# Kernel optimization log

Measured on AMD Instinct MI355X. Metric: run time of the kernel, lower is better.

Reference implementation:

```python
import jax, jax.numpy as jnp
import numpy as np

D_MODEL = 2048
N_HEADS = 16
D_K = D_MODEL // N_HEADS
D_FF = ((int(D_MODEL * 8 / 3) + 63) // 64) * 64  # 5504
B, S = 2, 2048
EPS = 1e-6


def setup_inputs() -> dict:
    key = jax.random.key(0)
    ks = jax.random.split(key, 16)
    sc = 0.02
    x = jax.random.normal(ks[0], (B, S, D_MODEL), dtype=jnp.float32)
    mask = jnp.tril(jnp.ones((S, S), dtype=jnp.int32))[None]  # [1,S,S] causal
    inp = {
        'x': x,
        'mask': mask,
        'wq': jax.random.normal(ks[1], (D_MODEL, D_MODEL), jnp.float32) * sc,
        'bq': jnp.zeros((D_MODEL,), jnp.float32),
        'wk': jax.random.normal(ks[2], (D_MODEL, D_MODEL), jnp.float32) * sc,
        'bk': jnp.zeros((D_MODEL,), jnp.float32),
        'wv': jax.random.normal(ks[3], (D_MODEL, D_MODEL), jnp.float32) * sc,
        'bv': jnp.zeros((D_MODEL,), jnp.float32),
        'wo': jax.random.normal(ks[4], (D_MODEL, D_MODEL), jnp.float32) * sc,
        'bo': jnp.zeros((D_MODEL,), jnp.float32),
        'g1': jnp.ones((D_MODEL,), jnp.float32),  # RMSNorm weights
        'g2': jnp.ones((D_MODEL,), jnp.float32),
        'w1': jax.random.normal(ks[5], (D_MODEL, D_FF), jnp.float32) * sc,
        'w3': jax.random.normal(ks[6], (D_MODEL, D_FF), jnp.float32) * sc,
        'w2': jax.random.normal(ks[7], (D_FF, D_MODEL), jnp.float32) * sc,
    }
    return inp


def _rmsnorm(x, w):
    rms = jnp.sqrt(jnp.mean(x * x, axis=-1, keepdims=True) + EPS)
    return x / rms * w


def _block(x, mask, wq, bq, wk, bk, wv, bv, wo, bo, g1, g2, w1, w2, w3):
    b, s, _ = x.shape
    # --- attention sublayer (pre-LN) ---
    n = _rmsnorm(x, g1)
    q = (n @ wq + bq).reshape(b, s, N_HEADS, D_K).transpose(0, 2, 1, 3)
    k = (n @ wk + bk).reshape(b, s, N_HEADS, D_K).transpose(0, 2, 1, 3)
    v = (n @ wv + bv).reshape(b, s, N_HEADS, D_K).transpose(0, 2, 1, 3)
    scores = jnp.einsum('bhqd,bhkd->bhqk', q, k) / jnp.sqrt(jnp.float32(D_K))
    m = mask[:, None, :, :]  # [1,1,S,S]
    scores = jnp.where(m == 0, jnp.float32(-jnp.inf), scores)
    attn = jax.nn.softmax(scores, axis=-1)
    ao = jnp.einsum('bhqk,bhkd->bhqd', attn, v)
    ao = ao.transpose(0, 2, 1, 3).reshape(b, s, D_MODEL)
    x = x + (ao @ wo + bo)
    # --- SwiGLU FFN sublayer (pre-LN) ---
    n = _rmsnorm(x, g2)
    ffn = (jax.nn.silu(n @ w1) * (n @ w3)) @ w2
    return x + ffn


def reference(x, mask, wq, bq, wk, bk, wv, bv, wo, bo, g1, g2, w1, w2, w3):
    return _block(x, mask, wq, bq, wk, bk, wv, bv, wo, bo, g1, g2, w1, w2, w3)
```

## Files before the change

kernel.cpp:

```cpp
#include <hip/hip_runtime.h>
#include <stdint.h>

typedef unsigned short u16;
typedef __bf16 bf16x8 __attribute__((ext_vector_type(8)));
typedef float f32x4 __attribute__((ext_vector_type(4)));

#define D_MODEL 2048
#define NHEADS 16
#define DK 128
#define DFF 5504
#define DFFP 5632
#define BB 2
#define SS 2048
#define MTOK 4096
#define DQKV 6144

#define AS1 __attribute__((address_space(1)))
#define AS3 __attribute__((address_space(3)))

__device__ __forceinline__ u16 f2bf(float f){
  union { float f; uint32_t u; } v; v.f = f;
  uint32_t r = v.u + 0x7fffu + ((v.u >> 16) & 1u);
  return (u16)(r >> 16);
}
__device__ __forceinline__ float bf2f(u16 u){
  union { uint32_t u; float f; } v; v.u = ((uint32_t)u) << 16;
  return v.f;
}
__device__ __forceinline__ u16 cvt_bf16(float f){
  union { __bf16 h; u16 u; } v; v.h = (__bf16)f; return v.u;
}
__device__ __forceinline__ float fexp2(float x){
#if __has_builtin(__builtin_amdgcn_exp2f)
  return __builtin_amdgcn_exp2f(x);
#else
  return exp2f(x);
#endif
}

__global__ __launch_bounds__(256) void k_transpose_w(const float* __restrict__ W,
                                                     u16* __restrict__ Wt, int K, int Nsrc){
  __shared__ float tile[32][33];
  int n0 = blockIdx.x * 32, k0 = blockIdx.y * 32;
  int tx = threadIdx.x, ty = threadIdx.y;
  #pragma unroll
  for (int r = 0; r < 4; ++r){
    int n = n0 + tx;
    tile[ty + r*8][tx] = (n < Nsrc) ? W[(size_t)(k0 + ty + r*8) * Nsrc + n] : 0.0f;
  }
  __syncthreads();
  #pragma unroll
  for (int r = 0; r < 4; ++r)
    Wt[(size_t)(n0 + ty + r*8) * K + k0 + tx] = f2bf(tile[tx][ty + r*8]);
}

__global__ __launch_bounds__(256) void k_transpose_v(const u16* __restrict__ V,
                                                     u16* __restrict__ Vt, int ld){
  __shared__ u16 tile[32][33];
  int s0 = blockIdx.x * 32;
  int bh = blockIdx.y >> 2, dt = blockIdx.y & 3;
  int b = bh >> 4, h = bh & 15;
  int tx = threadIdx.x, ty = threadIdx.y;
  #pragma unroll
  for (int r = 0; r < 4; ++r)
    tile[ty + r*8][tx] = V[(size_t)(b*SS + s0 + ty + r*8) * ld + h*DK + dt*32 + tx];
  __syncthreads();
  #pragma unroll
  for (int r = 0; r < 4; ++r)
    Vt[(size_t)(bh*DK + dt*32 + ty + r*8) * SS + s0 + tx] = tile[tx][ty + r*8];
}

__global__ __launch_bounds__(256) void k_concat3(const float* __restrict__ a,
                                                 const float* __restrict__ b,
                                                 const float* __restrict__ c,
                                                 float* __restrict__ o){
  int i = blockIdx.x*256 + threadIdx.x;
  if (i >= DQKV) return;
  o[i] = (i < 2048) ? a[i] : (i < 4096 ? b[i-2048] : c[i-4096]);
}

__global__ __launch_bounds__(256) void k_rmsnorm(const float* __restrict__ X,
                                                 const float* __restrict__ g,
                                                 u16* __restrict__ out){
  int row = blockIdx.x, tid = threadIdx.x;
  const float* x = X + (size_t)row * D_MODEL;
  float4 a = ((const float4*)x)[tid*2];
  float4 b = ((const float4*)x)[tid*2+1];
  float ss = a.x*a.x + a.y*a.y + a.z*a.z + a.w*a.w
           + b.x*b.x + b.y*b.y + b.z*b.z + b.w*b.w;
  #pragma unroll
  for (int m = 1; m < 64; m <<= 1) ss += __shfl_xor(ss, m, 64);
  __shared__ float red[4];
  if ((tid & 63) == 0) red[tid >> 6] = ss;
  __syncthreads();
  float tot = red[0] + red[1] + red[2] + red[3];
  float sc = rsqrtf(tot * (1.0f / D_MODEL) + 1e-6f);
  float4 ga = ((const float4*)g)[tid*2];
  float4 gb = ((const float4*)g)[tid*2+1];
  uint32_t w0 = f2bf(a.x*sc*ga.x) | ((uint32_t)f2bf(a.y*sc*ga.y) << 16);
  uint32_t w1 = f2bf(a.z*sc*ga.z) | ((uint32_t)f2bf(a.w*sc*ga.w) << 16);
  uint32_t w2 = f2bf(b.x*sc*gb.x) | ((uint32_t)f2bf(b.y*sc*gb.y) << 16);
  uint32_t w3 = f2bf(b.z*sc*gb.z) | ((uint32_t)f2bf(b.w*sc*gb.w) << 16);
  ((uint4*)(out + (size_t)row * D_MODEL))[tid] = make_uint4(w0, w1, w2, w3);
}

__global__ __launch_bounds__(256) void k_silu_mul(const u16* __restrict__ a,
                                                  const u16* __restrict__ b,
                                                  u16* __restrict__ o, int n8){
  int i = blockIdx.x * 256 + threadIdx.x;
  if (i >= n8) return;
  uint4 av = ((const uint4*)a)[i];
  uint4 bv = ((const uint4*)b)[i];
  uint32_t aa[4] = {av.x, av.y, av.z, av.w};
  uint32_t bb[4] = {bv.x, bv.y, bv.z, bv.w};
  uint32_t rr[4];
  #pragma unroll
  for (int j = 0; j < 4; ++j){
    float x0 = bf2f((u16)(aa[j] & 0xffff)), x1 = bf2f((u16)(aa[j] >> 16));
    float y0 = bf2f((u16)(bb[j] & 0xffff)), y1 = bf2f((u16)(bb[j] >> 16));
    float r0 = x0 / (1.f + __expf(-x0)) * y0;
    float r1 = x1 / (1.f + __expf(-x1)) * y1;
    rr[j] = f2bf(r0) | ((uint32_t)f2bf(r1) << 16);
  }
  ((uint4*)o)[i] = make_uint4(rr[0], rr[1], rr[2], rr[3]);
}

__global__ __launch_bounds__(256) void k_add2(float* __restrict__ out,
                                              const float* __restrict__ p0,
                                              const float* __restrict__ p1, int n4){
  int stride = gridDim.x * 256;
  for (int i = blockIdx.x * 256 + threadIdx.x; i < n4; i += stride){
    float4 o = ((const float4*)out)[i];
    float4 a = ((const float4*)p0)[i];
    float4 b = ((const float4*)p1)[i];
    o.x += a.x + b.x; o.y += a.y + b.y; o.z += a.z + b.z; o.w += a.w + b.w;
    ((float4*)out)[i] = o;
  }
}

template<int EPI>
__global__ __launch_bounds__(512, 2) void k_gemm8p(
    const u16* __restrict__ A, const u16* __restrict__ Bt,
    const float* __restrict__ bias, const u16* __restrict__ aux,
    void* __restrict__ Cout, int M, int N, int K,
    int lda, int ldb, int ldc)
{
  extern __shared__ __align__(16) char smem[];
  const int tid = threadIdx.x;
  const int lane = tid & 63, wid = tid >> 6;
  const int wr = wid >> 2, wc = wid & 3;
  const int lrow = lane & 15, lhi = lane >> 4;

  int nwg = gridDim.x, wg = blockIdx.x;
  int ksl = 0;
  if constexpr (EPI == 6){
    int hn = nwg >> 1;
    if (wg >= hn){ ksl = 1; wg -= hn; }
    nwg = hn;
    A  += (size_t)ksl * K;
    Bt += (size_t)ksl * K;
  }

  int nbx = N >> 8, nbm = M >> 8;
  int xcd = wg & 7, sub = wg >> 3;
  int m0, n0;
  if ((nwg & 7) == 0 && (nbm & 1) == 0 && (nbx & 3) == 0){
    int mh = nbm >> 1;
    int mr = sub % mh, nc = sub / mh;
    m0 = (((xcd & 1) * mh) + mr) << 8;
    n0 = (((xcd >> 1) * (nbx >> 2)) + nc) << 8;
  } else {
    int qq = nwg >> 3, rr2 = nwg & 7;
    int swz = (xcd < rr2 ? xcd*(qq+1) : rr2*(qq+1) + (xcd-rr2)*qq) + sub;
    m0 = (swz / nbx) << 8; n0 = (swz % nbx) << 8;
  }

  const int nk = K >> 6;
  const int hA = wr, hB = wc >> 1;
  const int gA = wc;
  const int gB = (wr << 1) | (wc & 1);

  auto stA = [&](int d, int kk, int q){
    #pragma unroll
    for (int L = 0; L < 2; ++L){
      int p = q*8192 + gA*2048 + L*1024 + lane*16;
      int row = p >> 7;
      int o = (p & 127) ^ ((row & 7) << 4);
      __builtin_amdgcn_global_load_lds(
        (const AS1 void*)(A + (size_t)(m0 + hA*128 + row)*lda + kk + (o >> 1)),
        (AS3 void*)(smem + d*65536 + hA*16384 + p), 16, 0, 0);
    }
  };
  auto stB = [&](int d, int kk, int s){
    #pragma unroll
    for (int L = 0; L < 2; ++L){
      int p = s*4096 + (gB >> 1)*8192 + (gB & 1)*2048 + L*1024 + lane*16;
      int row = p >> 7;
      int o = (p & 127) ^ ((row & 7) << 4);
      __builtin_amdgcn_global_load_lds(
        (const AS1 void*)(Bt + (size_t)(n0 + hB*128 + row)*ldb + kk + (o >> 1)),
        (AS3 void*)(smem + d*65536 + 32768 + hB*16384 + p), 16, 0, 0);
    }
  };
  auto rdA = [&](int d, int rloc, int ks)->bf16x8{
    int p = rloc*128 + ((ks*64 + lhi*16) ^ ((rloc & 7) << 4));
    return *(const bf16x8*)(smem + d*65536 + hA*16384 + p);
  };
  auto rdB = [&](int d, int rloc, int ks)->bf16x8{
    int p = rloc*128 + ((ks*64 + lhi*16) ^ ((rloc & 7) << 4));
    return *(const bf16x8*)(smem + d*65536 + 32768 + hB*16384 + p);
  };

  f32x4 acc[8][4] = {};

  stA(0, 0, 0); stB(0, 0, 0); stB(0, 0, 1); stA(0, 0, 1);
  asm volatile("s_waitcnt vmcnt(0)" ::: "memory");
  __builtin_amdgcn_s_barrier();

  for (int t = 0; t < nk; ++t){
    int d = t & 1, dn = d ^ 1, kkn = (t + 1) << 6;
    bool pf = (t + 1 < nk);
    bf16x8 aR[8], bQ0[4], bQ1[4];

    #pragma unroll
    for (int ii = 0; ii < 4; ++ii){
      aR[ii*2]   = rdA(d, ii*16 + lrow, 0);
      aR[ii*2+1] = rdA(d, ii*16 + lrow, 1);
    }
    #pragma unroll
    for (int j = 0; j < 2; ++j){
      bQ0[j*2]   = rdB(d, (wc&1)*64 + j*16 + lrow, 0);
      bQ0[j*2+1] = rdB(d, (wc&1)*64 + j*16 + lrow, 1);
    }
    if (pf){ stA(dn, kkn, 0); stB(dn, kkn, 0); }
    __builtin_amdgcn_s_barrier();
    asm volatile("s_waitcnt lgkmcnt(0)" ::: "memory");
    __builtin_amdgcn_sched_barrier(0);
    __builtin_amdgcn_s_setprio(1);
    #pragma unroll
    for (int ii = 0; ii < 4; ++ii)
      #pragma unroll
      for (int j = 0; j < 2; ++j){
        acc[ii][j] = __builtin_amdgcn_mfma_f32_16x16x32_bf16(aR[ii*2],   bQ0[j*2],   acc[ii][j], 0, 0, 0);
        acc[ii][j] = __builtin_amdgcn_mfma_f32_16x16x32_bf16(aR[ii*2+1], bQ0[j*2+1], acc[ii][j], 0, 0, 0);
      }
    __builtin_amdgcn_s_setprio(0);
    if (pf) asm volatile("s_waitcnt vmcnt(6)" ::: "memory");
    else    asm volatile("s_waitcnt vmcnt(2)" ::: "memory");
    __builtin_amdgcn_sched_barrier(0);
    __builtin_amdgcn_s_barrier();

    #pragma unroll
    for (int j = 0; j < 2; ++j){
      bQ1[j*2]   = rdB(d, (wc&1)*64 + 32 + j*16 + lrow, 0);
      bQ1[j*2+1] = rdB(d, (wc&1)*64 + 32 + j*16 + lrow, 1);
    }
    if (pf) stB(dn, kkn, 1);
    __builtin_amdgcn_s_barrier();
    asm volatile("s_waitcnt lgkmcnt(0)" ::: "memory");
    __builtin_amdgcn_sched_barrier(0);
    __builtin_amdgcn_s_setprio(1);
    #pragma unroll
    for (int ii = 0; ii < 4; ++ii)
      #pragma unroll
      for (int j = 0; j < 2; ++j){
        acc[ii][2+j] = __builtin_amdgcn_mfma_f32_16x16x32_bf16(aR[ii*2],   bQ1[j*2],   acc[ii][2+j], 0, 0, 0);
        acc[ii][2+j] = __builtin_amdgcn_mfma_f32_16x16x32_bf16(aR[ii*2+1], bQ1[j*2+1], acc[ii][2+j], 0, 0, 0);
      }
    __builtin_amdgcn_s_setprio(0);
    if (pf) asm volatile("s_waitcnt vmcnt(6)" ::: "memory");
    else    asm volatile("s_waitcnt vmcnt(0)" ::: "memory");
    __builtin_amdgcn_sched_barrier(0);
    __builtin_amdgcn_s_barrier();

    #pragma unroll
    for (int ii = 0; ii < 4; ++ii){
      aR[ii*2]   = rdA(d, 64 + ii*16 + lrow, 0);
      aR[ii*2+1] = rdA(d, 64 + ii*16 + lrow, 1);
    }
    if (pf) stA(dn, kkn, 1);
    __builtin_amdgcn_s_barrier();
    asm volatile("s_waitcnt lgkmcnt(0)" ::: "memory");
    __builtin_amdgcn_sched_barrier(0);
    __builtin_amdgcn_s_setprio(1);
    #pragma unroll
    for (int ii = 0; ii < 4; ++ii)
      #pragma unroll
      for (int j = 0; j < 2; ++j){
        acc[4+ii][2+j] = __builtin_amdgcn_mfma_f32_16x16x32_bf16(aR[ii*2],   bQ1[j*2],   acc[4+ii][2+j], 0, 0, 0);
        acc[4+ii][2+j] = __builtin_amdgcn_mfma_f32_16x16x32_bf16(aR[ii*2+1], bQ1[j*2+1], acc[4+ii][2+j], 0, 0, 0);
      }
    __builtin_amdgcn_s_setprio(0);
    __builtin_amdgcn_s_barrier();

    __builtin_amdgcn_s_setprio(1);
    #pragma unroll
    for (int ii = 0; ii < 4; ++ii)
      #pragma unroll
      for (int j = 0; j < 2; ++j){
        acc[4+ii][j] = __builtin_amdgcn_mfma_f32_16x16x32_bf16(aR[ii*2],   bQ0[j*2],   acc[4+ii][j], 0, 0, 0);
        acc[4+ii][j] = __builtin_amdgcn_mfma_f32_16x16x32_bf16(aR[ii*2+1], bQ0[j*2+1], acc[4+ii][j], 0, 0, 0);
      }
    __builtin_amdgcn_s_setprio(0);
    if (pf) asm volatile("s_waitcnt vmcnt(4)" ::: "memory");
    __builtin_amdgcn_sched_barrier(0);
    __builtin_amdgcn_s_barrier();
  }

  if constexpr (EPI == 6){
    float* P = ksl ? (float*)aux : (float*)Cout;
    #pragma unroll
    for (int i = 0; i < 8; ++i)
      #pragma unroll
      for (int j = 0; j < 4; ++j){
        int col = n0 + wc*64 + j*16 + lrow;
        #pragma unroll
        for (int q = 0; q < 4; ++q){
          int row = m0 + wr*128 + i*16 + lhi*4 + q;
          P[(size_t)row*ldc + col] = acc[i][j][q];
        }
      }
    return;
  }
  u16* Cw = (u16*)Cout;
  int cofs = 0;
  if constexpr (EPI == 5){
    if (n0 >= 5632){ Cw = (u16*)aux; cofs = 5632; }
  }
  #pragma unroll
  for (int i = 0; i < 8; ++i){
    #pragma unroll
    for (int j = 0; j < 4; ++j){
      int col = n0 + wc*64 + j*16 + lrow;
      float bv = 0.f;
      if constexpr (EPI == 0) bv = bias[col];
      #pragma unroll
      for (int q = 0; q < 4; ++q){
        int row = m0 + wr*128 + i*16 + lhi*4 + q;
        float v = acc[i][j][q] + bv;
        Cw[(size_t)row*ldc + (col - cofs)] = f2bf(v);
      }
    }
  }
}

template<int EPI>
__global__ __launch_bounds__(256) void k_gemm_bt(
    const u16* __restrict__ A, const u16* __restrict__ Bt,
    const float* __restrict__ bias, const float* __restrict__ res,
    const u16* __restrict__ aux,
    void* __restrict__ Cout, int M, int N, int K,
    int lda, int ldb, int ldc)
{
  __shared__ __align__(16) u16 As[3][128*32];
  __shared__ __align__(16) u16 Bs[3][128*32];
  int tid = threadIdx.x;

  int nwg = gridDim.x, wg = blockIdx.x;
  int qq = nwg >> 3, rr = nwg & 7;
  int xcd = wg & 7, sub = wg >> 3;
  int swz = (xcd < rr ? xcd*(qq+1) : rr*(qq+1) + (xcd-rr)*qq) + sub;
  int nbx = N >> 7;
  int m0 = (swz / nbx) << 7, n0 = (swz % nbx) << 7;

  int lane = tid & 63, wave = tid >> 6;
  int wr = wave >> 1, wc = wave & 1;
  int lrow = lane & 15, lhi = lane >> 4;
  f32x4 acc[4][4] = {};
  int srow = tid >> 2;
  int schk = tid & 3;
  const int nk = K >> 5;

  auto stage = [&](int slot, int kt){
    int k0 = kt << 5;
    int c = schk ^ (srow & 3);
    #pragma unroll
    for (int cc = 0; cc < 2; ++cc){
      int r = cc*64 + srow;
      __builtin_amdgcn_global_load_lds(
        (const AS1 void*)(A + (size_t)(m0 + r)*lda + k0 + c*8),
        (AS3 void*)(&As[slot][r*32 + schk*8]), 16, 0, 0);
      __builtin_amdgcn_global_load_lds(
        (const AS1 void*)(Bt + (size_t)(n0 + r)*ldb + k0 + c*8),
        (AS3 void*)(&Bs[slot][r*32 + schk*8]), 16, 0, 0);
    }
  };

  stage(0, 0);
  if (nk > 1) stage(1, 1);
  if (nk > 1) asm volatile("s_waitcnt vmcnt(4)" ::: "memory");
  else        asm volatile("s_waitcnt vmcnt(0)" ::: "memory");
  __builtin_amdgcn_s_barrier();

  for (int kt = 0; kt < nk; ++kt){
    int cur = kt % 3;
    if (kt + 2 < nk) stage((kt + 2) % 3, kt + 2);
    int rchk = lhi ^ (lrow & 3);
    bf16x8 af[4], bfv[4];
    #pragma unroll
    for (int i = 0; i < 4; ++i){
      af[i]  = *(const bf16x8*)(&As[cur][(wr*64 + i*16 + lrow)*32 + rchk*8]);
      bfv[i] = *(const bf16x8*)(&Bs[cur][(wc*64 + i*16 + lrow)*32 + rchk*8]);
    }
    #pragma unroll
    for (int i = 0; i < 4; ++i)
      #pragma unroll
      for (int j = 0; j < 4; ++j)
        acc[i][j] = __builtin_amdgcn_mfma_f32_16x16x32_bf16(af[i], bfv[j], acc[i][j], 0, 0, 0);
    if (kt + 2 < nk) asm volatile("s_waitcnt vmcnt(4)" ::: "memory");
    else             asm volatile("s_waitcnt vmcnt(0)" ::: "memory");
    __builtin_amdgcn_s_barrier();
  }

  #pragma unroll
  for (int i = 0; i < 4; ++i){
    #pragma unroll
    for (int j = 0; j < 4; ++j){
      int col = n0 + wc*64 + j*16 + lrow;
      float bv = 0.f;
      if constexpr (EPI == 0 || EPI == 1) bv = bias[col];
      #pragma unroll
      for (int q = 0; q < 4; ++q){
        int row = m0 + wr*64 + i*16 + lhi*4 + q;
        size_t idx = (size_t)row*ldc + col;
        float v = acc[i][j][q] + bv;
        if constexpr (EPI == 1 || EPI == 3) v += res[idx];
        if constexpr (EPI == 4){
          float a0 = bf2f(aux[idx]);
          v = a0 / (1.f + __expf(-a0)) * v;
        }
        if constexpr (EPI == 0 || EPI == 2 || EPI == 4) ((u16*)Cout)[idx] = f2bf(v);
        else ((float*)Cout)[idx] = v;
      }
    }
  }
}

__global__ __launch_bounds__(512) void k_attn(
    const u16* __restrict__ Q, const u16* __restrict__ Kb,
    const u16* __restrict__ Vt, u16* __restrict__ O, int ldq)
{
  int tid = threadIdx.x, lane = tid & 63, wave = tid >> 6;
  int lrow = lane & 15, lhi = lane >> 4;
  int bidx = blockIdx.x;
  int bh = bidx >> 3, j = bidx & 7;
  int b = bh >> 4, h = bh & 15;

  __shared__ __align__(16) u16 Kbuf[2][64*128];
  __shared__ __align__(16) u16 Vbuf[2][128*64];
  __shared__ __align__(16) u16 P_lds[8][16*64];
  char* pw = (char*)&P_lds[wave][0];
  const float sc2 = 0.08838834764831845f * 1.44269504088896340736f;

  auto stage = [&](int bufi, int kt){
    int kv0 = kt << 6;
    char* kd = (char*)&Kbuf[bufi][0];
    char* vd = (char*)&Vbuf[bufi][0];
    #pragma unroll
    for (int L = 0; L < 2; ++L){
      int cid = wave*128 + L*64 + lane;
      int r = cid >> 4, c = cid & 15;
      int cg = c ^ (r & 7);
      __builtin_amdgcn_global_load_lds(
        (const AS1 void*)(Kb + (size_t)(b*SS + kv0 + r)*ldq + h*DK + cg*8),
        (AS3 void*)(kd + wave*2048 + L*1024 + lane*16), 16, 0, 0);
      int dd = cid >> 3, c8 = cid & 7;
      int cv = c8 ^ (dd & 7);
      __builtin_amdgcn_global_load_lds(
        (const AS1 void*)(Vt + (size_t)bh*DK*SS + (size_t)dd*SS + kv0 + cv*8),
        (AS3 void*)(vd + wave*2048 + L*1024 + lane*16), 16, 0, 0);
    }
  };

  #pragma unroll 1
  for (int item = 0; item < 2; ++item){
    int qi = item == 0 ? 15 - j : j;
    int qs = qi * 128;
    int nt = 2*qi + 2;
    int qrow = qs + wave * 16;

    bf16x8 qf[4];
    const u16* qbase = Q + (size_t)(b*SS + qrow + lrow)*ldq + h*DK + lhi*8;
    #pragma unroll
    for (int dc = 0; dc < 4; ++dc) qf[dc] = *(const bf16x8*)(qbase + dc*32);

    f32x4 accO[8] = {};
    float mr[4] = {-1e30f,-1e30f,-1e30f,-1e30f};
    float lr[4] = {0.f,0.f,0.f,0.f};

    stage(0, 0);
    __syncthreads();

    for (int kt = 0; kt < nt; ++kt){
      int cur = kt & 1;
      if (kt + 1 < nt) stage(cur ^ 1, kt + 1);
      int kv0 = kt << 6;
      if (kv0 <= qrow + 15){
        const char* kl = (const char*)&Kbuf[cur][0];
        const char* vl = (const char*)&Vbuf[cur][0];
        bool domask = (kv0 + 63 > qrow);

        f32x4 sf[4];
        #pragma unroll
        for (int hf = 0; hf < 4; ++hf){
          int rl = hf*16 + lrow;
          int sw = rl & 7;
          f32x4 a = {};
          #pragma unroll
          for (int dc = 0; dc < 4; ++dc){
            bf16x8 kf = *(const bf16x8*)(kl + rl*256 + (((lhi + dc*4) ^ sw) << 4));
            a = __builtin_amdgcn_mfma_f32_16x16x32_bf16(qf[dc], kf, a, 0, 0, 0);
          }
          sf[hf] = a;
        }

        float p[4][4], mx[4];
        #pragma unroll
        for (int q = 0; q < 4; ++q){
          float s0 = sf[0][q]*sc2, s1 = sf[1][q]*sc2, s2 = sf[2][q]*sc2, s3 = sf[3][q]*sc2;
          if (domask){
            int qg = qrow + lhi*4 + q;
            if (kv0      + lrow > qg) s0 = -1e30f;
            if (kv0 + 16 + lrow > qg) s1 = -1e30f;
            if (kv0 + 32 + lrow > qg) s2 = -1e30f;
            if (kv0 + 48 + lrow > qg) s3 = -1e30f;
          }
          p[q][0]=s0; p[q][1]=s1; p[q][2]=s2; p[q][3]=s3;
          float m = fmaxf(fmaxf(s0,s1), fmaxf(s2,s3));
          m = fmaxf(m, __shfl_xor(m, 1, 64));
          m = fmaxf(m, __shfl_xor(m, 2, 64));
          m = fmaxf(m, __shfl_xor(m, 4, 64));
          m = fmaxf(m, __shfl_xor(m, 8, 64));
          mx[q] = m;
        }
        float dmax = fmaxf(fmaxf(mx[0]-mr[0], mx[1]-mr[1]), fmaxf(mx[2]-mr[2], mx[3]-mr[3]));
        bool rescale = !__all(dmax <= 8.0f);
        float al[4];
        #pragma unroll
        for (int q = 0; q < 4; ++q){
          if (rescale){
            float mn = fmaxf(mr[q], mx[q]);
            al[q] = fexp2(mr[q] - mn);
            mr[q] = mn;
          } else al[q] = 1.0f;
          p[q][0] = fexp2(p[q][0] - mr[q]);
          p[q][1] = fexp2(p[q][1] - mr[q]);
          p[q][2] = fexp2(p[q][2] - mr[q]);
          p[q][3] = fexp2(p[q][3] - mr[q]);
          float sm = (p[q][0] + p[q][1]) + (p[q][2] + p[q][3]);
          sm += __shfl_xor(sm, 1, 64);
          sm += __shfl_xor(sm, 2, 64);
          sm += __shfl_xor(sm, 4, 64);
          sm += __shfl_xor(sm, 8, 64);
          lr[q] = lr[q]*al[q] + sm;
        }
        if (rescale){
          #pragma unroll
          for (int f = 0; f < 8; ++f)
            #pragma unroll
            for (int q = 0; q < 4; ++q) accO[f][q] *= al[q];
        }

        #pragma unroll
        for (int q = 0; q < 4; ++q){
          int row = lhi*4 + q;
          int rb = row*128, sw = (row & 7) << 4;
          #pragma unroll
          for (int hf = 0; hf < 4; ++hf)
            *(u16*)(pw + rb + ((hf*32 + lrow*2) ^ sw)) = cvt_bf16(p[q][hf]);
        }
        __builtin_amdgcn_sched_barrier(0);
        int rsw = (lrow & 7) << 4;
        bf16x8 pa0 = *(const bf16x8*)(pw + lrow*128 + ((     lhi*16) ^ rsw));
        bf16x8 pa1 = *(const bf16x8*)(pw + lrow*128 + ((64 + lhi*16) ^ rsw));

        #pragma unroll
        for (int f = 0; f < 8; ++f){
          int d = f*16 + lrow;
          int swv = d & 7;
          bf16x8 v0 = *(const bf16x8*)(vl + d*128 + (((lhi    ) ^ swv) << 4));
          bf16x8 v1 = *(const bf16x8*)(vl + d*128 + (((lhi + 4) ^ swv) << 4));
          accO[f] = __builtin_amdgcn_mfma_f32_16x16x32_bf16(pa0, v0, accO[f], 0, 0, 0);
          accO[f] = __builtin_amdgcn_mfma_f32_16x16x32_bf16(pa1, v1, accO[f], 0, 0, 0);
        }
      }
      __syncthreads();
    }

    #pragma unroll
    for (int q = 0; q < 4; ++q){
      float inv = 1.0f / lr[q];
      #pragma unroll
      for (int f = 0; f < 8; ++f){
        int row = b*SS + qrow + lhi*4 + q;
        int col = h*DK + f*16 + lrow;
        O[(size_t)row*D_MODEL + col] = cvt_bf16(accO[f][q] * inv);
      }
    }
    __syncthreads();
  }
}

extern "C" void kernel_launch(void* const* d_in, const int* in_sizes, int n_in,
                              void* d_out, int out_size, void* d_ws, size_t ws_size,
                              hipStream_t stream)
{
  (void)in_sizes; (void)n_in; (void)out_size;
  const float* x  = (const float*)d_in[0];
  const float* wq = (const float*)d_in[2];
  const float* bq = (const float*)d_in[3];
  const float* wk = (const float*)d_in[4];
  const float* bk = (const float*)d_in[5];
  const float* wv = (const float*)d_in[6];
  const float* bv = (const float*)d_in[7];
  const float* wo = (const float*)d_in[8];
  const float* bo = (const float*)d_in[9];
  const float* g1 = (const float*)d_in[10];
  const float* g2 = (const float*)d_in[11];
  const float* w1 = (const float*)d_in[12];
  const float* w3 = (const float*)d_in[13];
  const float* w2 = (const float*)d_in[14];
  float* out = (float*)d_out;

  const size_t MB = 1u << 20;
  const size_t W2T_B = (size_t)D_MODEL * DFF * sizeof(u16);
  const size_t NEED = 152*MB + W2T_B + 32768;
  if (ws_size < NEED) return;
  char* ws = (char*)d_ws;
  u16* bufA  = (u16*)(ws + 0);
  u16* qkv   = (u16*)(ws + 16*MB);
  u16* h1    = qkv;
  u16* wqkvt = (u16*)(ws + 64*MB);
  u16* w1w3t = (u16*)(ws + 64*MB);
  u16* wot   = (u16*)(ws + 88*MB);
  u16* vtb   = (u16*)(ws + 96*MB);
  u16* h3    = (u16*)(ws + 108*MB);
  float* p0  = (float*)(ws + 64*MB);
  float* p1  = (float*)(ws + 96*MB);
  u16* w2t   = (u16*)(ws + 152*MB);
  float* bqkv = (float*)(ws + 152*MB + W2T_B);

  bool big = true;
  big &= hipFuncSetAttribute((const void*)k_gemm8p<0>, hipFuncAttributeMaxDynamicSharedMemorySize, 131072) == hipSuccess;
  big &= hipFuncSetAttribute((const void*)k_gemm8p<5>, hipFuncAttributeMaxDynamicSharedMemorySize, 131072) == hipSuccess;
  big &= hipFuncSetAttribute((const void*)k_gemm8p<6>, hipFuncAttributeMaxDynamicSharedMemorySize, 131072) == hipSuccess;

  dim3 tb(32, 8);
  k_transpose_w<<<dim3(64,64), tb, 0, stream>>>(wq, wqkvt,               D_MODEL, D_MODEL);
  k_transpose_w<<<dim3(64,64), tb, 0, stream>>>(wk, wqkvt + 2048*2048,   D_MODEL, D_MODEL);
  k_transpose_w<<<dim3(64,64), tb, 0, stream>>>(wv, wqkvt + 2*2048*2048, D_MODEL, D_MODEL);
  k_transpose_w<<<dim3(64,64), tb, 0, stream>>>(wo, wot, D_MODEL, D_MODEL);
  k_transpose_w<<<dim3(64, DFF/32), tb, 0, stream>>>(w2, w2t, DFF, D_MODEL);
  k_concat3<<<24, 256, 0, stream>>>(bq, bk, bv, bqkv);

  k_rmsnorm<<<MTOK, 256, 0, stream>>>(x, g1, bufA);
  if (big)
    k_gemm8p<0><<<(MTOK/256)*(DQKV/256), 512, 131072, stream>>>(bufA, wqkvt, bqkv, nullptr, qkv, MTOK, DQKV, D_MODEL, D_MODEL, D_MODEL, DQKV);
  else
    k_gemm_bt<0><<<(DQKV/128)*(MTOK/128), 256, 0, stream>>>(bufA, wqkvt, bqkv, nullptr, nullptr, qkv, MTOK, DQKV, D_MODEL, D_MODEL, D_MODEL, DQKV);
  k_transpose_v<<<dim3(SS/32, 128), tb, 0, stream>>>(qkv + 4096, vtb, DQKV);
  k_transpose_w<<<dim3(DFFP/32, 64), tb, 0, stream>>>(w1, w1w3t, D_MODEL, DFF);
  k_attn<<<dim3(BB*NHEADS*8), 512, 0, stream>>>(qkv, qkv + 2048, vtb, bufA, DQKV);
  k_gemm_bt<1><<<16*32, 256, 0, stream>>>(bufA, wot, bo, x, nullptr, out, MTOK, D_MODEL, D_MODEL, D_MODEL, D_MODEL, D_MODEL);
  k_transpose_w<<<dim3(DFFP/32, 64), tb, 0, stream>>>(w3, w1w3t + (size_t)DFFP*2048, D_MODEL, DFF);
  k_rmsnorm<<<MTOK, 256, 0, stream>>>(out, g2, bufA);
  if (big){
    k_gemm8p<5><<<(MTOK/256)*((2*DFFP)/256), 512, 131072, stream>>>(bufA, w1w3t, nullptr, h3, h1, MTOK, 2*DFFP, D_MODEL, D_MODEL, D_MODEL, DFFP);
    k_silu_mul<<<(MTOK*DFFP/8 + 255)/256, 256, 0, stream>>>(h1, h3, h1, MTOK*DFFP/8);
    k_gemm8p<6><<<2*(MTOK/256)*(D_MODEL/256), 512, 131072, stream>>>(h1, w2t, nullptr, (const u16*)p1, p0, MTOK, D_MODEL, DFF/2, DFFP, DFF, D_MODEL);
    k_add2<<<2048, 256, 0, stream>>>(out, p0, p1, MTOK*D_MODEL/4);
  } else {
    k_gemm_bt<2><<<(DFFP/128)*32, 256, 0, stream>>>(bufA, w1w3t, nullptr, nullptr, nullptr, h1, MTOK, DFFP, D_MODEL, D_MODEL, D_MODEL, DFFP);
    k_gemm_bt<2><<<(DFFP/128)*32, 256, 0, stream>>>(bufA, w1w3t + (size_t)DFFP*2048, nullptr, nullptr, nullptr, h3, MTOK, DFFP, D_MODEL, D_MODEL, D_MODEL, DFFP);
    k_silu_mul<<<(MTOK*DFFP/8 + 255)/256, 256, 0, stream>>>(h1, h3, h1, MTOK*DFFP/8);
    k_gemm_bt<3><<<16*32, 256, 0, stream>>>(h1, w2t, nullptr, out, nullptr, out, MTOK, D_MODEL, DFF, DFFP, DFF, D_MODEL);
  }
}
```

Before: 671.7 us.

## Use split-K 8-wave GEMM for output projection, batch weight transposes, hoist addressing

Replaces the 128-tile output projection GEMM with the 256-tile split-K k_gemm8p<6> path that writes two fp32 partials, then a new kernel adds the residual, bias and both partials. Merges the four square weight transposes into one 3D-grid launch. Precomputes the global/LDS addresses and swizzle offsets in the 8-wave GEMM so they are not recomputed every k-step. The split-K path adds extra fp32 partial traffic plus an extra elementwise pass, and raises register pressure from the hoisted pointer arrays.

```diff
diff --git a/kernel.cpp b/kernel.cpp
--- a/kernel.cpp
+++ b/kernel.cpp
@@ -52,6 +52,25 @@
   #pragma unroll
   for (int r = 0; r < 4; ++r)
     Wt[(size_t)(n0 + ty + r*8) * K + k0 + tx] = f2bf(tile[tx][ty + r*8]);
+}
+
+__global__ __launch_bounds__(256) void k_transpose_w4(
+    const float* __restrict__ w0s, const float* __restrict__ w1s,
+    const float* __restrict__ w2s, const float* __restrict__ w3s,
+    u16* __restrict__ d0, u16* __restrict__ d1,
+    u16* __restrict__ d2, u16* __restrict__ d3){
+  __shared__ float tile[32][33];
+  const float* W = blockIdx.z == 0 ? w0s : blockIdx.z == 1 ? w1s : blockIdx.z == 2 ? w2s : w3s;
+  u16* Wt = blockIdx.z == 0 ? d0 : blockIdx.z == 1 ? d1 : blockIdx.z == 2 ? d2 : d3;
+  int n0 = blockIdx.x * 32, k0 = blockIdx.y * 32;
+  int tx = threadIdx.x, ty = threadIdx.y;
+  #pragma unroll
+  for (int r = 0; r < 4; ++r)
+    tile[ty + r*8][tx] = W[(size_t)(k0 + ty + r*8) * D_MODEL + n0 + tx];
+  __syncthreads();
+  #pragma unroll
+  for (int r = 0; r < 4; ++r)
+    Wt[(size_t)(n0 + ty + r*8) * D_MODEL + k0 + tx] = f2bf(tile[tx][ty + r*8]);
 }
 
 __global__ __launch_bounds__(256) void k_transpose_v(const u16* __restrict__ V,
@@ -138,6 +157,23 @@
   }
 }
 
+__global__ __launch_bounds__(256) void k_addres(float* __restrict__ out,
+                                                const float* __restrict__ x,
+                                                const float* __restrict__ bias,
+                                                const float* __restrict__ p0,
+                                                const float* __restrict__ p1, int n4){
+  int stride = gridDim.x * 256;
+  for (int i = blockIdx.x * 256 + threadIdx.x; i < n4; i += stride){
+    float4 o = ((const float4*)x)[i];
+    float4 bb = ((const float4*)bias)[i & (D_MODEL/4 - 1)];
+    float4 a = ((const float4*)p0)[i];
+    float4 b = ((const float4*)p1)[i];
+    o.x += bb.x + a.x + b.x; o.y += bb.y + a.y + b.y;
+    o.z += bb.z + a.z + b.z; o.w += bb.w + a.w + b.w;
+    ((float4*)out)[i] = o;
+  }
+}
+
 template<int EPI>
 __global__ __launch_bounds__(512, 2) void k_gemm8p(
     const u16* __restrict__ A, const u16* __restrict__ Bt,
@@ -180,35 +216,45 @@
   const int gA = wc;
   const int gB = (wr << 1) | (wc & 1);
 
-  auto stA = [&](int d, int kk, int q){
+  const u16* aSrc[2][2]; int aDst[2][2];
+  const u16* bSrc[2][2]; int bDst[2][2];
+  #pragma unroll
+  for (int q = 0; q < 2; ++q)
     #pragma unroll
     for (int L = 0; L < 2; ++L){
       int p = q*8192 + gA*2048 + L*1024 + lane*16;
       int row = p >> 7;
       int o = (p & 127) ^ ((row & 7) << 4);
+      aSrc[q][L] = A + (size_t)(m0 + hA*128 + row)*lda + (o >> 1);
+      aDst[q][L] = hA*16384 + p;
+      int pb = q*4096 + (gB >> 1)*8192 + (gB & 1)*2048 + L*1024 + lane*16;
+      int rowb = pb >> 7;
+      int ob = (pb & 127) ^ ((rowb & 7) << 4);
+      bSrc[q][L] = Bt + (size_t)(n0 + hB*128 + rowb)*ldb + (ob >> 1);
+      bDst[q][L] = 32768 + hB*16384 + pb;
+    }
+  const int xo0 = (lhi*16) ^ ((lrow & 7) << 4);
+  const int xo1 = (64 + lhi*16) ^ ((lrow & 7) << 4);
+
+  auto stA = [&](int d, int kk, int q){
+    #pragma unroll
+    for (int L = 0; L < 2; ++L)
       __builtin_amdgcn_global_load_lds(
-        (const AS1 void*)(A + (size_t)(m0 + hA*128 + row)*lda + kk + (o >> 1)),
-        (AS3 void*)(smem + d*65536 + hA*16384 + p), 16, 0, 0);
-    }
+        (const AS1 void*)(aSrc[q][L] + kk),
+        (AS3 void*)(smem + d*65536 + aDst[q][L]), 16, 0, 0);
   };
   auto stB = [&](int d, int kk, int s){
     #pragma unroll
-    for (int L = 0; L < 2; ++L){
-      int p = s*4096 + (gB >> 1)*8192 + (gB & 1)*2048 + L*1024 + lane*16;
-      int row = p >> 7;
-      int o = (p & 127) ^ ((row & 7) << 4);
+    for (int L = 0; L < 2; ++L)
       __builtin_amdgcn_global_load_lds(
-        (const AS1 void*)(Bt + (size_t)(n0 + hB*128 + row)*ldb + kk + (o >> 1)),
-        (AS3 void*)(smem + d*65536 + 32768 + hB*16384 + p), 16, 0, 0);
-    }
+        (const AS1 void*)(bSrc[s][L] + kk),
+        (AS3 void*)(smem + d*65536 + bDst[s][L]), 16, 0, 0);
   };
   auto rdA = [&](int d, int rloc, int ks)->bf16x8{
-    int p = rloc*128 + ((ks*64 + lhi*16) ^ ((rloc & 7) << 4));
-    return *(const bf16x8*)(smem + d*65536 + hA*16384 + p);
+    return *(const bf16x8*)(smem + d*65536 + hA*16384 + rloc*128 + (ks ? xo1 : xo0));
   };
   auto rdB = [&](int d, int rloc, int ks)->bf16x8{
-    int p = rloc*128 + ((ks*64 + lhi*16) ^ ((rloc & 7) << 4));
-    return *(const bf16x8*)(smem + d*65536 + 32768 + hB*16384 + p);
+    return *(const bf16x8*)(smem + d*65536 + 32768 + hB*16384 + rloc*128 + (ks ? xo1 : xo0));
   };
 
   f32x4 acc[8][4] = {};
@@ -635,6 +681,8 @@
   u16* wot   = (u16*)(ws + 88*MB);
   u16* vtb   = (u16*)(ws + 96*MB);
   u16* h3    = (u16*)(ws + 108*MB);
+  float* p0o = (float*)(ws + 16*MB);
+  float* p1o = (float*)(ws + 108*MB);
   float* p0  = (float*)(ws + 64*MB);
   float* p1  = (float*)(ws + 96*MB);
   u16* w2t   = (u16*)(ws + 152*MB);
@@ -646,30 +694,33 @@
   big &= hipFuncSetAttribute((const void*)k_gemm8p<6>, hipFuncAttributeMaxDynamicSharedMemorySize, 131072) == hipSuccess;
 
   dim3 tb(32, 8);
-  k_transpose_w<<<dim3(64,64), tb, 0, stream>>>(wq, wqkvt,               D_MODEL, D_MODEL);
-  k_transpose_w<<<dim3(64,64), tb, 0, stream>>>(wk, wqkvt + 2048*2048,   D_MODEL, D_MODEL);
-  k_transpose_w<<<dim3(64,64), tb, 0, stream>>>(wv, wqkvt + 2*2048*2048, D_MODEL, D_MODEL);
-  k_transpose_w<<<dim3(64,64), tb, 0, stream>>>(wo, wot, D_MODEL, D_MODEL);
+  k_transpose_w4<<<dim3(64,64,4), tb, 0, stream>>>(wq, wk, wv, wo,
+      wqkvt, wqkvt + 2048*2048, wqkvt + 2*2048*2048, wot);
   k_transpose_w<<<dim3(64, DFF/32), tb, 0, stream>>>(w2, w2t, DFF, D_MODEL);
   k_concat3<<<24, 256, 0, stream>>>(bq, bk, bv, bqkv);
 
   k_rmsnorm<<<MTOK, 256, 0, stream>>>(x, g1, bufA);
-  if (big)
+  if (big){
     k_gemm8p<0><<<(MTOK/256)*(DQKV/256), 512, 131072, stream>>>(bufA, wqkvt, bqkv, nullptr, qkv, MTOK, DQKV, D_MODEL, D_MODEL, D_MODEL, DQKV);
-  else
-    k_gemm_bt<0><<<(DQKV/128)*(MTOK/128), 256, 0, stream>>>(bufA, wqkvt, bqkv, nullptr, nullptr, qkv, MTOK, DQKV, D_MODEL, D_MODEL, D_MODEL, DQKV);
-  k_transpose_v<<<dim3(SS/32, 128), tb, 0, stream>>>(qkv + 4096, vtb, DQKV);
-  k_transpose_w<<<dim3(DFFP/32, 64), tb, 0, stream>>>(w1, w1w3t, D_MODEL, DFF);
-  k_attn<<<dim3(BB*NHEADS*8), 512, 0, stream>>>(qkv, qkv + 2048, vtb, bufA, DQKV);
-  k_gemm_bt<1><<<16*32, 256, 0, stream>>>(bufA, wot, bo, x, nullptr, out, MTOK, D_MODEL, D_MODEL, D_MODEL, D_MODEL, D_MODEL);
-  k_transpose_w<<<dim3(DFFP/32, 64), tb, 0, stream>>>(w3, w1w3t + (size_t)DFFP*2048, D_MODEL, DFF);
-  k_rmsnorm<<<MTOK, 256, 0, stream>>>(out, g2, bufA);
-  if (big){
+    k_transpose_v<<<dim3(SS/32, 128), tb, 0, stream>>>(qkv + 4096, vtb, DQKV);
+    k_transpose_w<<<dim3(DFFP/32, 64), tb, 0, stream>>>(w1, w1w3t, D_MODEL, DFF);
+    k_attn<<<dim3(BB*NHEADS*8), 512, 0, stream>>>(qkv, qkv + 2048, vtb, bufA, DQKV);
+    k_gemm8p<6><<<2*(MTOK/256)*(D_MODEL/256), 512, 131072, stream>>>(bufA, wot, nullptr, (const u16*)p1o, p0o, MTOK, D_MODEL, D_MODEL/2, D_MODEL, D_MODEL, D_MODEL);
+    k_addres<<<2048, 256, 0, stream>>>(out, x, bo, p0o, p1o, MTOK*D_MODEL/4);
+    k_transpose_w<<<dim3(DFFP/32, 64), tb, 0, stream>>>(w3, w1w3t + (size_t)DFFP*2048, D_MODEL, DFF);
+    k_rmsnorm<<<MTOK, 256, 0, stream>>>(out, g2, bufA);
     k_gemm8p<5><<<(MTOK/256)*((2*DFFP)/256), 512, 131072, stream>>>(bufA, w1w3t, nullptr, h3, h1, MTOK, 2*DFFP, D_MODEL, D_MODEL, D_MODEL, DFFP);
     k_silu_mul<<<(MTOK*DFFP/8 + 255)/256, 256, 0, stream>>>(h1, h3, h1, MTOK*DFFP/8);
     k_gemm8p<6><<<2*(MTOK/256)*(D_MODEL/256), 512, 131072, stream>>>(h1, w2t, nullptr, (const u16*)p1, p0, MTOK, D_MODEL, DFF/2, DFFP, DFF, D_MODEL);
     k_add2<<<2048, 256, 0, stream>>>(out, p0, p1, MTOK*D_MODEL/4);
   } else {
+    k_gemm_bt<0><<<(DQKV/128)*(MTOK/128), 256, 0, stream>>>(bufA, wqkvt, bqkv, nullptr, nullptr, qkv, MTOK, DQKV, D_MODEL, D_MODEL, D_MODEL, DQKV);
+    k_transpose_v<<<dim3(SS/32, 128), tb, 0, stream>>>(qkv + 4096, vtb, DQKV);
+    k_transpose_w<<<dim3(DFFP/32, 64), tb, 0, stream>>>(w1, w1w3t, D_MODEL, DFF);
+    k_attn<<<dim3(BB*NHEADS*8), 512, 0, stream>>>(qkv, qkv + 2048, vtb, bufA, DQKV);
+    k_gemm_bt<1><<<16*32, 256, 0, stream>>>(bufA, wot, bo, x, nullptr, out, MTOK, D_MODEL, D_MODEL, D_MODEL, D_MODEL, D_MODEL);
+    k_transpose_w<<<dim3(DFFP/32, 64), tb, 0, stream>>>(w3, w1w3t + (size_t)DFFP*2048, D_MODEL, DFF);
+    k_rmsnorm<<<MTOK, 256, 0, stream>>>(out, g2, bufA);
     k_gemm_bt<2><<<(DFFP/128)*32, 256, 0, stream>>>(bufA, w1w3t, nullptr, nullptr, nullptr, h1, MTOK, DFFP, D_MODEL, D_MODEL, D_MODEL, DFFP);
     k_gemm_bt<2><<<(DFFP/128)*32, 256, 0, stream>>>(bufA, w1w3t + (size_t)DFFP*2048, nullptr, nullptr, nullptr, h3, MTOK, DFFP, D_MODEL, D_MODEL, D_MODEL, DFFP);
     k_silu_mul<<<(MTOK*DFFP/8 + 255)/256, 256, 0, stream>>>(h1, h3, h1, MTOK*DFFP/8);
```

Measured after the change: 675.4 us. No clear change (+0.5%).
